# Kernel optimization log

Measured on AMD Instinct MI355X. Metric: run time of the kernel, lower is better.

Reference implementation:

```python
import jax, jax.numpy as jnp
import numpy as np

B, T, D, H, L, V = 2, 1024, 1024, 16, 4, 32000
HS = D // H  # head_size = 64


def setup_inputs() -> dict:
    key = jax.random.key(0)
    ks = jax.random.split(key, 15)
    s = 0.02
    return {
        "idx": jax.random.randint(ks[0], (B, T), 0, V, dtype=jnp.int32),
        "tok_emb": jax.random.normal(ks[1], (V, D), jnp.float32) * s,
        "pos_emb": jax.random.normal(ks[2], (T, D), jnp.float32) * s,
        "Wq": jax.random.normal(ks[3], (L, H, D, HS), jnp.float32) * s,
        "Wk": jax.random.normal(ks[4], (L, H, D, HS), jnp.float32) * s,
        "Wv": jax.random.normal(ks[5], (L, H, D, HS), jnp.float32) * s,
        "Wproj": jax.random.normal(ks[6], (L, D, D), jnp.float32) * s,
        "bproj": jnp.zeros((L, D), jnp.float32),
        "W1": jax.random.normal(ks[7], (L, D, 4 * D), jnp.float32) * s,
        "b1": jnp.zeros((L, 4 * D), jnp.float32),
        "W2": jax.random.normal(ks[8], (L, 4 * D, D), jnp.float32) * s,
        "b2": jnp.zeros((L, D), jnp.float32),
        "Wlm": jax.random.normal(ks[9], (D, V), jnp.float32) * s,
        "blm": jnp.zeros((V,), jnp.float32),
    }


def reference(idx, tok_emb, pos_emb, Wq, Wk, Wv, Wproj, bproj, W1, b1, W2, b2, Wlm, blm):
    Bn, Tn = idx.shape
    Dn = tok_emb.shape[1]
    x = tok_emb[idx] + pos_emb[jnp.arange(Tn)][None, :, :]  # (B,T,D)
    causal = jnp.tril(jnp.ones((Tn, Tn), dtype=bool))
    # NOTE: original scales by C**-0.5 where C = embedding_dim (not head_size)
    scale = Dn ** -0.5
    n_layers = Wq.shape[0]
    for l in range(n_layers):
        q = jnp.einsum('btd,hdk->bhtk', x, Wq[l])
        k = jnp.einsum('btd,hdk->bhtk', x, Wk[l])
        v = jnp.einsum('btd,hdk->bhtk', x, Wv[l])
        scores = jnp.einsum('bhtk,bhsk->bhts', q, k) * scale
        scores = jnp.where(causal[None, None, :, :], scores, -jnp.inf)
        probs = jax.nn.softmax(scores, axis=-1)
        attn = jnp.einsum('bhts,bhsk->bhtk', probs, v)
        # concat heads in head order -> (B,T,H*HS)
        attn = attn.transpose(0, 2, 1, 3).reshape(Bn, Tn, Dn)
        x = x + attn @ Wproj[l] + bproj[l]
        h = jax.nn.relu(x @ W1[l] + b1[l])
        x = x + h @ W2[l] + b2[l]
    return x @ Wlm + blm  # (B,T,V) logits
```

## Files before the change

kernel.cpp:

```cpp
#include <hip/hip_runtime.h>
#include <stdint.h>

#define DEVI static __device__ __forceinline__

typedef __attribute__((ext_vector_type(8))) _Float16  f16x8;
typedef __attribute__((ext_vector_type(8))) uint16_t  u16x8;
typedef __attribute__((ext_vector_type(4))) uint16_t  u16x4;
typedef __attribute__((ext_vector_type(4))) float     f32x4;

DEVI uint16_t f2h(float f){ return __builtin_bit_cast(uint16_t, (_Float16)f); }

DEVI void gload_lds16(const void* g, void* l){
  __builtin_amdgcn_global_load_lds((__attribute__((address_space(1))) void*)g,
                                   (__attribute__((address_space(3))) void*)l, 16, 0, 0);
}
DEVI f16x8 frag_ld(const void* base, int byteoff){
  const u16x8* p = (const u16x8*)((const char*)base + byteoff);
  return __builtin_bit_cast(f16x8, *p);
}

__global__ __launch_bounds__(256) void transpose_f32_f16(
    const float* __restrict__ in, uint16_t* __restrict__ out,
    int ld_in, int ld_out,
    long long in_z, long long out_zA, long long out_zB, int zdiv)
{
  __shared__ float tile[64][65];
  const int r0 = blockIdx.x * 64, c0 = blockIdx.y * 64;
  const int z  = blockIdx.z;
  const float* inp = in + (long long)z * in_z;
  uint16_t* outp = out + (long long)(z / zdiv) * out_zA + (long long)(z % zdiv) * out_zB;
  const int tx = threadIdx.x & 63, ty = threadIdx.x >> 6;
  #pragma unroll
  for (int i = 0; i < 16; i++){
    int r = i * 4 + ty;
    tile[r][tx] = inp[(long long)(r0 + r) * ld_in + (c0 + tx)];
  }
  __syncthreads();
  const int rp = (threadIdx.x & 31) * 2;
  const int cy = threadIdx.x >> 5;
  #pragma unroll
  for (int i = 0; i < 8; i++){
    int c = i * 8 + cy;
    uint32_t v = (uint32_t)f2h(tile[rp][c]) | ((uint32_t)f2h(tile[rp + 1][c]) << 16);
    *(uint32_t*)(outp + (long long)(c0 + c) * ld_out + (r0 + rp)) = v;
  }
}

__global__ __launch_bounds__(256) void embed_kernel(
    const int* __restrict__ idx, const float* __restrict__ tok,
    const float* __restrict__ pos, float* __restrict__ xf, uint16_t* __restrict__ xb)
{
  const int t = blockIdx.x;
  const int d = threadIdx.x * 4;
  const int token = idx[t];
  const int tp = t & 1023;
  const float4 tv = *(const float4*)(tok + (size_t)token * 1024 + d);
  const float4 pv = *(const float4*)(pos + (size_t)tp * 1024 + d);
  float4 s; s.x = tv.x + pv.x; s.y = tv.y + pv.y; s.z = tv.z + pv.z; s.w = tv.w + pv.w;
  *(float4*)(xf + (size_t)t * 1024 + d) = s;
  uint16_t* o = xb + (size_t)t * 1024 + d;
  o[0] = f2h(s.x); o[1] = f2h(s.y); o[2] = f2h(s.z); o[3] = f2h(s.w);
}

template<bool SPLITK, bool BIAS, bool RELU, bool OUTF, bool OUTB, bool QSCALE>
__global__ __launch_bounds__(256, 3) void gemm_bt(
    const uint16_t* __restrict__ A, const uint16_t* __restrict__ Bt,
    const float* __restrict__ bias,
    float* __restrict__ outf, uint16_t* __restrict__ outb,
    int M, int N, int K)
{
  __shared__ __align__(16) uint16_t As[128 * 64];
  __shared__ __align__(16) uint16_t Bs[128 * 64];
  const int tid = threadIdx.x, lane = tid & 63, wid = tid >> 6;

  const int Mt = M >> 7;
  int flat = blockIdx.x;
  int kidx = 0;
  if constexpr (SPLITK){ kidx = flat & 1; flat >>= 1; }
  const int total = SPLITK ? (gridDim.x >> 1) : gridDim.x;
  const int wg = (flat & 7) * (total >> 3) + (flat >> 3);
  const int bm = (wg % Mt) * 128, bn = (wg / Mt) * 128;
  int k0 = 0, k1 = K;
  if constexpr (SPLITK){ const int Kh = K >> 1; k0 = kidx * Kh; k1 = k0 + Kh; }
  float* outp = outf;
  if constexpr (SPLITK) outp = outf + (size_t)kidx * M * N;

  const uint16_t* gA[4]; const uint16_t* gB[4];
  #pragma unroll
  for (int i = 0; i < 4; i++){
    int c = i * 256 + tid;
    int row = c >> 3;
    int p = (c * 16) ^ ((row & 7) << 4);
    int off = (p >> 1) & 63;
    gA[i] = A  + (size_t)(bm + row) * K + off;
    gB[i] = Bt + (size_t)(bn + row) * K + off;
  }

  f32x4 acc[4][4];
  const f32x4 fz = {0.f, 0.f, 0.f, 0.f};
  #pragma unroll
  for (int a = 0; a < 4; a++)
    #pragma unroll
    for (int n = 0; n < 4; n++) acc[a][n] = fz;

  const int lrow = lane & 15, lk2 = (lane >> 4) * 16;
  const int wr = (wid >> 1) * 64, wc = (wid & 1) * 64;

  for (int kt = k0; kt < k1; kt += 64){
    #pragma unroll
    for (int i = 0; i < 4; i++)
      gload_lds16(gA[i] + kt, (char*)As + (i * 256 + wid * 64) * 16);
    #pragma unroll
    for (int i = 0; i < 4; i++)
      gload_lds16(gB[i] + kt, (char*)Bs + (i * 256 + wid * 64) * 16);
    __syncthreads();
    #pragma unroll
    for (int kk = 0; kk < 2; kk++){
      f16x8 af[4], bfv[4];
      #pragma unroll
      for (int mf = 0; mf < 4; mf++){
        int row = wr + mf * 16 + lrow;
        af[mf] = frag_ld(As, (row * 128 + kk * 64 + lk2) ^ ((row & 7) << 4));
      }
      #pragma unroll
      for (int nf = 0; nf < 4; nf++){
        int row = wc + nf * 16 + lrow;
        bfv[nf] = frag_ld(Bs, (row * 128 + kk * 64 + lk2) ^ ((row & 7) << 4));
      }
      #pragma unroll
      for (int mf = 0; mf < 4; mf++)
        #pragma unroll
        for (int nf = 0; nf < 4; nf++)
          acc[mf][nf] = __builtin_amdgcn_mfma_f32_16x16x32_f16(af[mf], bfv[nf], acc[mf][nf], 0, 0, 0);
    }
    __syncthreads();
  }

  #pragma unroll
  for (int mf = 0; mf < 4; mf++){
    const int row0 = bm + wr + mf * 16 + (lane >> 4) * 4;
    #pragma unroll
    for (int nf = 0; nf < 4; nf++){
      const int col = bn + wc + nf * 16 + (lane & 15);
      float bv = 0.f;
      if constexpr (BIAS) bv = bias[col];
      float qs = 1.0f;
      if constexpr (QSCALE) qs = (col < 1024) ? 0.03125f : 1.0f;
      #pragma unroll
      for (int j = 0; j < 4; j++){
        float v = acc[mf][nf][j] + bv;
        size_t oi = (size_t)(row0 + j) * N + col;
        if constexpr (RELU) v = fmaxf(v, 0.f);
        if constexpr (OUTF) outp[oi] = v;
        if constexpr (OUTB) outb[oi] = f2h(v * qs);
      }
    }
  }
}

__global__ __launch_bounds__(256, 2) void gemm_lm(
    const uint16_t* __restrict__ A, const uint16_t* __restrict__ Bt,
    const float* __restrict__ bias, float* __restrict__ outf,
    int M, int N, int K)
{
  __shared__ __align__(16) uint16_t As[128 * 64];
  __shared__ __align__(16) uint16_t Bs[256 * 64];
  const int tid = threadIdx.x, lane = tid & 63, wid = tid >> 6;

  const int Mt = M >> 7;
  const int flat = blockIdx.x;
  const int wg = (flat & 7) * (gridDim.x >> 3) + (flat >> 3);
  const int bm = (wg % Mt) * 128, bn = (wg / Mt) * 256;

  const uint16_t* gA[4]; const uint16_t* gB[8];
  #pragma unroll
  for (int i = 0; i < 4; i++){
    int c = i * 256 + tid;
    int row = c >> 3;
    int p = (c * 16) ^ ((row & 7) << 4);
    int off = (p >> 1) & 63;
    gA[i] = A + (size_t)(bm + row) * K + off;
  }
  #pragma unroll
  for (int i = 0; i < 8; i++){
    int c = i * 256 + tid;
    int row = c >> 3;
    int p = (c * 16) ^ ((row & 7) << 4);
    int off = (p >> 1) & 63;
    gB[i] = Bt + (size_t)(bn + row) * K + off;
  }

  f32x4 acc[4][8];
  const f32x4 fz = {0.f, 0.f, 0.f, 0.f};
  #pragma unroll
  for (int a = 0; a < 4; a++)
    #pragma unroll
    for (int n = 0; n < 8; n++) acc[a][n] = fz;

  const int lrow = lane & 15, lk2 = (lane >> 4) * 16;
  const int wr = (wid >> 1) * 64, wc = (wid & 1) * 128;

  for (int kt = 0; kt < K; kt += 64){
    #pragma unroll
    for (int i = 0; i < 4; i++)
      gload_lds16(gA[i] + kt, (char*)As + (i * 256 + wid * 64) * 16);
    #pragma unroll
    for (int i = 0; i < 8; i++)
      gload_lds16(gB[i] + kt, (char*)Bs + (i * 256 + wid * 64) * 16);
    __syncthreads();
    #pragma unroll
    for (int kk = 0; kk < 2; kk++){
      f16x8 af[4], bfv[8];
      #pragma unroll
      for (int mf = 0; mf < 4; mf++){
        int row = wr + mf * 16 + lrow;
        af[mf] = frag_ld(As, (row * 128 + kk * 64 + lk2) ^ ((row & 7) << 4));
      }
      #pragma unroll
      for (int nf = 0; nf < 8; nf++){
        int row = wc + nf * 16 + lrow;
        bfv[nf] = frag_ld(Bs, (row * 128 + kk * 64 + lk2) ^ ((row & 7) << 4));
      }
      #pragma unroll
      for (int mf = 0; mf < 4; mf++)
        #pragma unroll
        for (int nf = 0; nf < 8; nf++)
          acc[mf][nf] = __builtin_amdgcn_mfma_f32_16x16x32_f16(af[mf], bfv[nf], acc[mf][nf], 0, 0, 0);
    }
    __syncthreads();
  }

  #pragma unroll
  for (int mf = 0; mf < 4; mf++){
    const int row0 = bm + wr + mf * 16 + (lane >> 4) * 4;
    #pragma unroll
    for (int nf = 0; nf < 8; nf++){
      const int col = bn + wc + nf * 16 + (lane & 15);
      const float bv = bias[col];
      #pragma unroll
      for (int j = 0; j < 4; j++)
        outf[(size_t)(row0 + j) * N + col] = acc[mf][nf][j] + bv;
    }
  }
}

__global__ __launch_bounds__(256) void reduce_sk(
    const float* __restrict__ p, const float* __restrict__ bias,
    float* __restrict__ xf, uint16_t* __restrict__ xb, int MN, int N)
{
  const int i = (blockIdx.x * 256 + threadIdx.x) * 4;
  const float4 a = *(const float4*)(p + i);
  const float4 b = *(const float4*)(p + MN + i);
  const int col = i & (N - 1);
  const float4 bv = *(const float4*)(bias + col);
  float4 x = *(float4*)(xf + i);
  x.x += a.x + b.x + bv.x;
  x.y += a.y + b.y + bv.y;
  x.z += a.z + b.z + bv.z;
  x.w += a.w + b.w + bv.w;
  *(float4*)(xf + i) = x;
  uint16_t* o = xb + i;
  o[0] = f2h(x.x); o[1] = f2h(x.y); o[2] = f2h(x.z); o[3] = f2h(x.w);
}

__global__ __launch_bounds__(256, 2) void attn_kernel(
    const uint16_t* __restrict__ qkv, uint16_t* __restrict__ out)
{
  const int bi = blockIdx.x;
  const int b  = bi >> 8;
  const int jj = bi & 255;
  const int h  = jj >> 4;
  int q64 = jj & 15;
  if (b) q64 = 15 - q64;

  __shared__ __align__(16) uint16_t Qs[64 * 64];
  __shared__ __align__(16) uint16_t Ks[128 * 64];
  __shared__ __align__(16) uint16_t Vt[64 * 128];
  __shared__ __align__(16) uint16_t Ps[64 * 128];

  const int tid = threadIdx.x, lane = tid & 63, wid = tid >> 6;
  const size_t bt0 = (size_t)b * 1024;

  int rowC[4], offC[4];
  #pragma unroll
  for (int i = 0; i < 4; i++){
    int c = i * 256 + tid;
    int row = c >> 3;
    int p = (c * 16) ^ ((row & 7) << 4);
    rowC[i] = row; offC[i] = (p >> 1) & 63;
  }

  #pragma unroll
  for (int i = 0; i < 2; i++)
    gload_lds16(qkv + (bt0 + q64 * 64 + rowC[i]) * 3072 + h * 64 + offC[i],
                (char*)Qs + (i * 256 + wid * 64) * 16);
  __syncthreads();

  const int lrow = lane & 15, lk2 = (lane >> 4) * 16, g4 = (lane >> 4) * 4;

  f16x8 aq[2];
  {
    int row = wid * 16 + lrow;
    #pragma unroll
    for (int kk = 0; kk < 2; kk++)
      aq[kk] = frag_ld(Qs, (row * 128 + kk * 64 + lk2) ^ ((row & 7) << 4));
  }

  float l_run[4];
  f32x4 acc_o[4];
  const f32x4 fz = {0.f, 0.f, 0.f, 0.f};
  #pragma unroll
  for (int j = 0; j < 4; j++){ l_run[j] = 0.f; acc_o[j] = fz; }

  const int tpV = (tid >> 4) * 2, d0V = (tid & 15) * 4;
  const int nkt = q64 >> 1;

  for (int kt = 0; kt <= nkt; ++kt){
    __syncthreads();
    #pragma unroll
    for (int i = 0; i < 4; i++)
      gload_lds16(qkv + (bt0 + kt * 128 + rowC[i]) * 3072 + 1024 + h * 64 + offC[i],
                  (char*)Ks + (i * 256 + wid * 64) * 16);
    #pragma unroll
    for (int i = 0; i < 4; i++){
      const int t = i * 32 + tpV;
      const uint16_t* src = qkv + (bt0 + kt * 128 + t) * 3072 + 2048 + h * 64 + d0V;
      const u16x4 v0 = *(const u16x4*)src;
      const u16x4 v1 = *(const u16x4*)(src + 3072);
      #pragma unroll
      for (int dd = 0; dd < 4; dd++){
        const int d = d0V + dd;
        const int byte = (d * 256 + t * 2) ^ ((((d >> 3) ^ d) & 15) << 4);
        *(uint32_t*)((char*)Vt + byte) = (uint32_t)v0[dd] | ((uint32_t)v1[dd] << 16);
      }
    }
    __syncthreads();

    f32x4 sf[8];
    #pragma unroll
    for (int n = 0; n < 8; n++) sf[n] = fz;
    __builtin_amdgcn_s_setprio(1);
    #pragma unroll
    for (int kk = 0; kk < 2; kk++){
      #pragma unroll
      for (int nf = 0; nf < 8; nf++){
        const int row = nf * 16 + lrow;
        const f16x8 bk = frag_ld(Ks, (row * 128 + kk * 64 + lk2) ^ ((row & 7) << 4));
        sf[nf] = __builtin_amdgcn_mfma_f32_16x16x32_f16(aq[kk], bk, sf[nf], 0, 0, 0);
      }
    }
    __builtin_amdgcn_s_setprio(0);

    const bool diag = (kt == nkt);
    #pragma unroll
    for (int j = 0; j < 4; j++){
      float ps = 0.f;
      if (diag){
        const int rg = q64 * 64 + wid * 16 + g4 + j;
        #pragma unroll
        for (int nf = 0; nf < 8; nf++){
          const int cg = kt * 128 + nf * 16 + lrow;
          const float p = (cg <= rg) ? __expf(sf[nf][j]) : 0.f;
          sf[nf][j] = p;
          ps += p;
        }
      } else {
        #pragma unroll
        for (int nf = 0; nf < 8; nf++){
          const float p = __expf(sf[nf][j]);
          sf[nf][j] = p;
          ps += p;
        }
      }
      #pragma unroll
      for (int mk = 1; mk < 16; mk <<= 1) ps += __shfl_xor(ps, mk);
      l_run[j] += ps;
      const int rl = wid * 16 + g4 + j;
      const int sw = (((rl >> 3) ^ rl) & 15) << 4;
      #pragma unroll
      for (int nf = 0; nf < 8; nf++){
        const int byte = (rl * 256 + (nf * 16 + lrow) * 2) ^ sw;
        *(uint16_t*)((char*)Ps + byte) = f2h(sf[nf][j]);
      }
    }
    __syncthreads();

    __builtin_amdgcn_s_setprio(1);
    #pragma unroll
    for (int kk = 0; kk < 4; kk++){
      const int row = wid * 16 + lrow;
      const f16x8 pa = frag_ld(Ps, (row * 256 + kk * 64 + lk2) ^ ((((row >> 3) ^ row) & 15) << 4));
      #pragma unroll
      for (int nh = 0; nh < 4; nh++){
        const int n = nh * 16 + lrow;
        const f16x8 vb = frag_ld(Vt, (n * 256 + kk * 64 + lk2) ^ ((((n >> 3) ^ n) & 15) << 4));
        acc_o[nh] = __builtin_amdgcn_mfma_f32_16x16x32_f16(pa, vb, acc_o[nh], 0, 0, 0);
      }
    }
    __builtin_amdgcn_s_setprio(0);
  }

  #pragma unroll
  for (int j = 0; j < 4; j++){
    const float inv = 1.f / l_run[j];
    const int rg = q64 * 64 + wid * 16 + g4 + j;
    #pragma unroll
    for (int nh = 0; nh < 4; nh++)
      out[(bt0 + rg) * 1024 + h * 64 + nh * 16 + lrow] = f2h(acc_o[nh][j] * inv);
  }
}

extern "C" void kernel_launch(void* const* d_in, const int* in_sizes, int n_in,
                              void* d_out, int out_size, void* d_ws, size_t ws_size,
                              hipStream_t stream)
{
  const int*   idx   = (const int*)  d_in[0];
  const float* tok   = (const float*)d_in[1];
  const float* pos   = (const float*)d_in[2];
  const float* Wq    = (const float*)d_in[3];
  const float* Wk    = (const float*)d_in[4];
  const float* Wv    = (const float*)d_in[5];
  const float* Wproj = (const float*)d_in[6];
  const float* bproj = (const float*)d_in[7];
  const float* W1    = (const float*)d_in[8];
  const float* b1    = (const float*)d_in[9];
  const float* W2    = (const float*)d_in[10];
  const float* b2    = (const float*)d_in[11];
  const float* Wlm   = (const float*)d_in[12];
  const float* blm   = (const float*)d_in[13];
  float* out = (float*)d_out;

  char* ws = (char*)d_ws;
  size_t off = 0;
  auto alloc = [&](size_t bytes){ void* p = ws + off; off += (bytes + 255) & ~(size_t)255; return p; };
  uint16_t* qkvT   = (uint16_t*)alloc((size_t)4 * 3072 * 1024 * 2);
  uint16_t* WprojT = (uint16_t*)alloc((size_t)4 * 1024 * 1024 * 2);
  uint16_t* W1T    = (uint16_t*)alloc((size_t)4 * 4096 * 1024 * 2);
  uint16_t* W2T    = (uint16_t*)alloc((size_t)4 * 1024 * 4096 * 2);
  uint16_t* WlmT   = (uint16_t*)alloc((size_t)32000 * 1024 * 2);
  float*    xf     = (float*)   alloc((size_t)2048 * 1024 * 4);
  uint16_t* xb     = (uint16_t*)alloc((size_t)2048 * 1024 * 2);
  uint16_t* qkv_a  = (uint16_t*)alloc((size_t)2048 * 3072 * 2);
  uint16_t* attnb  = (uint16_t*)alloc((size_t)2048 * 1024 * 2);
  uint16_t* hb     = (uint16_t*)alloc((size_t)2048 * 4096 * 2);
  float*    psum   = (float*)   alloc((size_t)2 * 2048 * 1024 * 4);
  (void)ws_size; (void)in_sizes; (void)n_in; (void)out_size;

  const dim3 tb(256);
  const int MN = 2048 * 1024;

  transpose_f32_f16<<<dim3(16, 1, 64), tb, 0, stream>>>(Wq, qkvT,                 64, 1024,
      65536LL, 3072LL * 1024, 64LL * 1024, 16);
  transpose_f32_f16<<<dim3(16, 1, 64), tb, 0, stream>>>(Wk, qkvT + 1024 * 1024,   64, 1024,
      65536LL, 3072LL * 1024, 64LL * 1024, 16);
  transpose_f32_f16<<<dim3(16, 1, 64), tb, 0, stream>>>(Wv, qkvT + 2048 * 1024,   64, 1024,
      65536LL, 3072LL * 1024, 64LL * 1024, 16);
  transpose_f32_f16<<<dim3(16, 16, 4), tb, 0, stream>>>(Wproj, WprojT, 1024, 1024,
      1048576LL, 1048576LL, 0LL, 1);
  transpose_f32_f16<<<dim3(16, 64, 4), tb, 0, stream>>>(W1, W1T, 4096, 1024,
      4194304LL, 4194304LL, 0LL, 1);
  transpose_f32_f16<<<dim3(64, 16, 4), tb, 0, stream>>>(W2, W2T, 1024, 4096,
      4194304LL, 4194304LL, 0LL, 1);
  transpose_f32_f16<<<dim3(16, 500, 1), tb, 0, stream>>>(Wlm, WlmT, 32000, 1024,
      0LL, 0LL, 0LL, 1);

  embed_kernel<<<dim3(2048), tb, 0, stream>>>(idx, tok, pos, xf, xb);

  for (int l = 0; l < 4; ++l){
    const uint16_t* qkvT_l = qkvT + (size_t)l * 3072 * 1024;
    gemm_bt<false, false, false, false, true, true><<<dim3(384), tb, 0, stream>>>(
        xb, qkvT_l, nullptr, nullptr, qkv_a, 2048, 3072, 1024);
    attn_kernel<<<dim3(512), tb, 0, stream>>>(qkv_a, attnb);
    gemm_bt<true, false, false, true, false, false><<<dim3(256), tb, 0, stream>>>(
        attnb, WprojT + (size_t)l * 1048576, nullptr, psum, nullptr, 2048, 1024, 1024);
    reduce_sk<<<dim3(2048), tb, 0, stream>>>(psum, bproj + l * 1024, xf, xb, MN, 1024);
    gemm_bt<false, true, true, false, true, false><<<dim3(512), tb, 0, stream>>>(
        xb, W1T + (size_t)l * 4194304, b1 + l * 4096, nullptr, hb, 2048, 4096, 1024);
    gemm_bt<true, false, false, true, false, false><<<dim3(256), tb, 0, stream>>>(
        hb, W2T + (size_t)l * 4194304, nullptr, psum, nullptr, 2048, 1024, 4096);
    reduce_sk<<<dim3(2048), tb, 0, stream>>>(psum, b2 + l * 1024, xf, xb, MN, 1024);
  }

  gemm_lm<<<dim3(2000), tb, 0, stream>>>(xb, WlmT, blm, out, 2048, 32000, 1024);
}
```

Baseline: 901.2 us.

## Fuse proj residual epilogue, widen transpose/V loads, defer softmax row-sum shuffle

The attention-projection GEMM now runs without split-K and adds bias and the residual in its epilogue, writing xf and xb directly. That removes one reduce kernel and the partial-sum traffic per layer, but the GEMM launches only 128 blocks, so the GPU is less full. The weight transpose reads float4 instead of scalars, and the attention V staging uses 16-byte loads. The per-tile row-sum shuffle reduction in attention moves to once after the loop, which is valid because the sums are linear.

```diff
diff --git a/kernel.cpp b/kernel.cpp
--- a/kernel.cpp
+++ b/kernel.cpp
@@ -29,11 +29,12 @@
   const int z  = blockIdx.z;
   const float* inp = in + (long long)z * in_z;
   uint16_t* outp = out + (long long)(z / zdiv) * out_zA + (long long)(z % zdiv) * out_zB;
-  const int tx = threadIdx.x & 63, ty = threadIdx.x >> 6;
-  #pragma unroll
-  for (int i = 0; i < 16; i++){
-    int r = i * 4 + ty;
-    tile[r][tx] = inp[(long long)(r0 + r) * ld_in + (c0 + tx)];
+  const int r16 = threadIdx.x >> 4, c4 = (threadIdx.x & 15) * 4;
+  #pragma unroll
+  for (int i = 0; i < 4; i++){
+    int r = i * 16 + r16;
+    const float4 v = *(const float4*)(inp + (long long)(r0 + r) * ld_in + (c0 + c4));
+    tile[r][c4] = v.x; tile[r][c4 + 1] = v.y; tile[r][c4 + 2] = v.z; tile[r][c4 + 3] = v.w;
   }
   __syncthreads();
   const int rp = (threadIdx.x & 31) * 2;
@@ -62,10 +63,10 @@
   o[0] = f2h(s.x); o[1] = f2h(s.y); o[2] = f2h(s.z); o[3] = f2h(s.w);
 }
 
-template<bool SPLITK, bool BIAS, bool RELU, bool OUTF, bool OUTB, bool QSCALE>
+template<bool SPLITK, bool BIAS, bool RELU, bool RES, bool OUTF, bool OUTB, bool QSCALE>
 __global__ __launch_bounds__(256, 3) void gemm_bt(
     const uint16_t* __restrict__ A, const uint16_t* __restrict__ Bt,
-    const float* __restrict__ bias,
+    const float* __restrict__ bias, const float* __restrict__ res,
     float* __restrict__ outf, uint16_t* __restrict__ outb,
     int M, int N, int K)
 {
@@ -150,6 +151,7 @@
       for (int j = 0; j < 4; j++){
         float v = acc[mf][nf][j] + bv;
         size_t oi = (size_t)(row0 + j) * N + col;
+        if constexpr (RES)  v += res[oi];
         if constexpr (RELU) v = fmaxf(v, 0.f);
         if constexpr (OUTF) outp[oi] = v;
         if constexpr (OUTB) outb[oi] = f2h(v * qs);
@@ -312,7 +314,7 @@
   #pragma unroll
   for (int j = 0; j < 4; j++){ l_run[j] = 0.f; acc_o[j] = fz; }
 
-  const int tpV = (tid >> 4) * 2, d0V = (tid & 15) * 4;
+  const int tpV = (tid >> 3) * 2, d0V = (tid & 7) * 8;
   const int nkt = q64 >> 1;
 
   for (int kt = 0; kt <= nkt; ++kt){
@@ -322,13 +324,13 @@
       gload_lds16(qkv + (bt0 + kt * 128 + rowC[i]) * 3072 + 1024 + h * 64 + offC[i],
                   (char*)Ks + (i * 256 + wid * 64) * 16);
     #pragma unroll
-    for (int i = 0; i < 4; i++){
-      const int t = i * 32 + tpV;
+    for (int i = 0; i < 2; i++){
+      const int t = i * 64 + tpV;
       const uint16_t* src = qkv + (bt0 + kt * 128 + t) * 3072 + 2048 + h * 64 + d0V;
-      const u16x4 v0 = *(const u16x4*)src;
-      const u16x4 v1 = *(const u16x4*)(src + 3072);
-      #pragma unroll
-      for (int dd = 0; dd < 4; dd++){
+      const u16x8 v0 = *(const u16x8*)src;
+      const u16x8 v1 = *(const u16x8*)(src + 3072);
+      #pragma unroll
+      for (int dd = 0; dd < 8; dd++){
         const int d = d0V + dd;
         const int byte = (d * 256 + t * 2) ^ ((((d >> 3) ^ d) & 15) << 4);
         *(uint32_t*)((char*)Vt + byte) = (uint32_t)v0[dd] | ((uint32_t)v1[dd] << 16);
@@ -372,8 +374,6 @@
           ps += p;
         }
       }
-      #pragma unroll
-      for (int mk = 1; mk < 16; mk <<= 1) ps += __shfl_xor(ps, mk);
       l_run[j] += ps;
       const int rl = wid * 16 + g4 + j;
       const int sw = (((rl >> 3) ^ rl) & 15) << 4;
@@ -398,6 +398,12 @@
       }
     }
     __builtin_amdgcn_s_setprio(0);
+  }
+
+  #pragma unroll
+  for (int j = 0; j < 4; j++){
+    #pragma unroll
+    for (int mk = 1; mk < 16; mk <<= 1) l_run[j] += __shfl_xor(l_run[j], mk);
   }
 
   #pragma unroll
@@ -468,16 +474,15 @@
 
   for (int l = 0; l < 4; ++l){
     const uint16_t* qkvT_l = qkvT + (size_t)l * 3072 * 1024;
-    gemm_bt<false, false, false, false, true, true><<<dim3(384), tb, 0, stream>>>(
-        xb, qkvT_l, nullptr, nullptr, qkv_a, 2048, 3072, 1024);
+    gemm_bt<false, false, false, false, false, true, true><<<dim3(384), tb, 0, stream>>>(
+        xb, qkvT_l, nullptr, nullptr, nullptr, qkv_a, 2048, 3072, 1024);
     attn_kernel<<<dim3(512), tb, 0, stream>>>(qkv_a, attnb);
-    gemm_bt<true, false, false, true, false, false><<<dim3(256), tb, 0, stream>>>(
-        attnb, WprojT + (size_t)l * 1048576, nullptr, psum, nullptr, 2048, 1024, 1024);
-    reduce_sk<<<dim3(2048), tb, 0, stream>>>(psum, bproj + l * 1024, xf, xb, MN, 1024);
-    gemm_bt<false, true, true, false, true, false><<<dim3(512), tb, 0, stream>>>(
-        xb, W1T + (size_t)l * 4194304, b1 + l * 4096, nullptr, hb, 2048, 4096, 1024);
-    gemm_bt<true, false, false, true, false, false><<<dim3(256), tb, 0, stream>>>(
-        hb, W2T + (size_t)l * 4194304, nullptr, psum, nullptr, 2048, 1024, 4096);
+    gemm_bt<false, true, false, true, true, true, false><<<dim3(128), tb, 0, stream>>>(
+        attnb, WprojT + (size_t)l * 1048576, bproj + l * 1024, xf, xf, xb, 2048, 1024, 1024);
+    gemm_bt<false, true, true, false, false, true, false><<<dim3(512), tb, 0, stream>>>(
+        xb, W1T + (size_t)l * 4194304, b1 + l * 4096, nullptr, nullptr, hb, 2048, 4096, 1024);
+    gemm_bt<true, false, false, false, true, false, false><<<dim3(256), tb, 0, stream>>>(
+        hb, W2T + (size_t)l * 4194304, nullptr, nullptr, psum, nullptr, 2048, 1024, 4096);
     reduce_sk<<<dim3(2048), tb, 0, stream>>>(psum, b2 + l * 1024, xf, xb, MN, 1024);
   }
 
```

After: 905.7 us (median of 2 runs). No clear change (+0.5%).
